# Optimization experiments

Measured on AMD Instinct MI355X. Metric: run time of the kernel, lower is better.

Reference implementation:

```python
import jax, jax.numpy as jnp
import numpy as np

DIM = 512
NUM_HEADS = 8
HEAD_DIM = DIM // NUM_HEADS


def setup_inputs() -> dict:
    key = jax.random.key(0)
    ks = jax.random.split(key, 9)
    s = 1.0 / np.sqrt(DIM)
    x = jax.random.normal(ks[0], (2, 4096, DIM), dtype=jnp.float32)
    Wq = jax.random.uniform(ks[1], (DIM, DIM), jnp.float32, -s, s)
    bq = jax.random.uniform(ks[2], (DIM,), jnp.float32, -s, s)
    Wk = jax.random.uniform(ks[3], (DIM, DIM), jnp.float32, -s, s)
    bk = jax.random.uniform(ks[4], (DIM,), jnp.float32, -s, s)
    Wv = jax.random.uniform(ks[5], (DIM, DIM), jnp.float32, -s, s)
    bv = jax.random.uniform(ks[6], (DIM,), jnp.float32, -s, s)
    Wo = jax.random.uniform(ks[7], (DIM, DIM), jnp.float32, -s, s)
    bo = jax.random.uniform(ks[8], (DIM,), jnp.float32, -s, s)
    return {"x": x, "Wq": Wq, "bq": bq, "Wk": Wk, "bk": bk,
            "Wv": Wv, "bv": bv, "Wo": Wo, "bo": bo}


def reference(x, Wq, bq, Wk, bk, Wv, bv, Wo, bo):
    B, S, D = x.shape
    H, Hd = NUM_HEADS, HEAD_DIM
    # Linear layers (torch stores weight as [out,in]; here W is [in,out])
    q = (x @ Wq + bq).reshape(B, S, H, Hd).transpose(0, 2, 1, 3)  # [B,H,S,Hd]
    k = (x @ Wk + bk).reshape(B, S, H, Hd).transpose(0, 2, 1, 3)
    v = (x @ Wv + bv).reshape(B, S, H, Hd).transpose(0, 2, 1, 3)
    # NOTE: original scales by dim**0.5, not head_dim**0.5
    energy = jnp.einsum('bhqd,bhkd->bhqk', q, k) / jnp.sqrt(jnp.float32(D))
    attn = jax.nn.softmax(energy, axis=-1)
    out = jnp.einsum('bhqk,bhkd->bhqd', attn, v)
    out = out.transpose(0, 2, 1, 3).reshape(B, S, D)
    return out @ Wo + bo
```

## Files before the change

kernel.cpp:

```cpp
#include <hip/hip_runtime.h>

typedef unsigned short USH;
typedef short s16x8 __attribute__((ext_vector_type(8)));
typedef float f32x4 __attribute__((ext_vector_type(4)));
typedef float f32x4v __attribute__((ext_vector_type(4)));
typedef unsigned int u32x4 __attribute__((ext_vector_type(4)));
typedef s16x8 s16x8_a __attribute__((may_alias));
typedef f32x4v f32x4v_a __attribute__((may_alias));
typedef u32x4 u32x4_a __attribute__((may_alias));
typedef unsigned long long u64_a __attribute__((may_alias));

#if __has_builtin(__builtin_amdgcn_exp2f)
#define EXP2F(x) __builtin_amdgcn_exp2f(x)
#else
#define EXP2F(x) __builtin_exp2f(x)
#endif

__device__ __forceinline__ USH f2bf(float f) {
  union { float f; unsigned int i; } c; c.f = f;
  unsigned int x = c.i;
  return (USH)((x + 0x7FFFu + ((x >> 16) & 1u)) >> 16);
}
__device__ __forceinline__ unsigned int pk_bf16(float a, float b) {
#if __has_builtin(__builtin_amdgcn_cvt_pk_bf16_f32)
  typedef USH ush2 __attribute__((ext_vector_type(2)));
  union { ush2 v; unsigned int u; } r;
  r.v = __builtin_amdgcn_cvt_pk_bf16_f32(a, b);
  return r.u;
#else
  union { float f; unsigned int i; } ca, cb; ca.f = a; cb.f = b;
  return ((ca.i + 0x8000u) >> 16) | ((cb.i + 0x8000u) & 0xFFFF0000u);
#endif
}

__device__ __forceinline__ f32x4 mfma16(s16x8 a, s16x8 b, f32x4 c) {
  return __builtin_amdgcn_mfma_f32_16x16x32_bf16(a, b, c, 0, 0, 0);
}

__global__ void transpose_w(const float* __restrict__ Wq, const float* __restrict__ Wk,
                            const float* __restrict__ Wv, const float* __restrict__ Wo,
                            USH* __restrict__ wsT) {
  __shared__ float tile[32][33];
  const int z = blockIdx.z;
  const float* W = (z == 0) ? Wq : (z == 1) ? Wk : (z == 2) ? Wv : Wo;
  USH* WT = wsT + (size_t)z * 262144;
  const int n0 = blockIdx.x * 32, k0 = blockIdx.y * 32;
  const int tx = threadIdx.x, ty = threadIdx.y;
  #pragma unroll
  for (int i = 0; i < 4; ++i)
    tile[ty + i * 8][tx] = W[(size_t)(k0 + ty + i * 8) * 512 + n0 + tx];
  __syncthreads();
  #pragma unroll
  for (int i = 0; i < 4; ++i)
    WT[(size_t)(n0 + ty + i * 8) * 512 + k0 + tx] = f2bf(tile[tx][ty + i * 8]);
}

__global__ __launch_bounds__(256) void cvt_x(const float* __restrict__ x,
                                             USH* __restrict__ xb) {
  const size_t i = ((size_t)blockIdx.x * 256 + threadIdx.x) * 8;
  const f32x4v a = *(const f32x4v_a*)(x + i);
  const f32x4v b = *(const f32x4v_a*)(x + i + 4);
  u32x4 s;
  s.x = pk_bf16(a.x, a.y); s.y = pk_bf16(a.z, a.w);
  s.z = pk_bf16(b.x, b.y); s.w = pk_bf16(b.z, b.w);
  *(u32x4_a*)(xb + i) = s;
}

template <int MODE>
__global__ __launch_bounds__(256, 3) void gemm_bias(
    const USH* __restrict__ A, const USH* __restrict__ BT0,
    const float* __restrict__ b0, const float* __restrict__ b1,
    const float* __restrict__ b2,
    USH* __restrict__ oQ, USH* __restrict__ oKV, float* __restrict__ oF) {
  __shared__ __align__(16) USH As[128 * 68];
  __shared__ __align__(16) USH Bs[128 * 68];
  const int z = blockIdx.z;
  const USH* BT = BT0 + (size_t)z * 262144;
  const float* bias = (z == 0) ? b0 : ((z == 1) ? b1 : b2);
  USH* outb = (z == 0) ? oQ : (oKV + (size_t)(z - 1) * 4194304);
  const float qs = (MODE == 1 && z == 0) ? 0.06375871528132839f : 1.0f;

  const int t = threadIdx.x;
  const int w = t >> 6, lane = t & 63;
  const int c = lane & 15, g = lane >> 4;
  const int wm = w & 1, wn = w >> 1;
  const int m0 = blockIdx.x * 128, n0 = blockIdx.y * 128;
  const int srow = t >> 1, scol = (t & 1) * 32;

  f32x4 acc[4][4] = {};

  const USH* Ap0 = A + (size_t)(m0 + srow) * 512 + scol;
  const USH* Bp0 = BT + (size_t)(n0 + srow) * 512 + scol;
  s16x8 pa[4], pb[4];
  #pragma unroll
  for (int j = 0; j < 4; ++j) {
    pa[j] = *(const s16x8_a*)(Ap0 + j * 8);
    pb[j] = *(const s16x8_a*)(Bp0 + j * 8);
  }

  for (int kt = 0; kt < 8; ++kt) {
    __syncthreads();
    #pragma unroll
    for (int j = 0; j < 4; ++j) {
      *(s16x8_a*)(As + srow * 68 + scol + j * 8) = pa[j];
      *(s16x8_a*)(Bs + srow * 68 + scol + j * 8) = pb[j];
    }
    const int ktn = (kt < 7) ? kt + 1 : kt;
    #pragma unroll
    for (int j = 0; j < 4; ++j) {
      pa[j] = *(const s16x8_a*)(Ap0 + ktn * 64 + j * 8);
      pb[j] = *(const s16x8_a*)(Bp0 + ktn * 64 + j * 8);
    }
    __syncthreads();
    #pragma unroll
    for (int ks = 0; ks < 2; ++ks) {
      s16x8 af[4], bfr[4];
      #pragma unroll
      for (int i = 0; i < 4; ++i) {
        af[i]  = *(const s16x8_a*)(As + (wm * 64 + i * 16 + c) * 68 + ks * 32 + g * 8);
        bfr[i] = *(const s16x8_a*)(Bs + (wn * 64 + i * 16 + c) * 68 + ks * 32 + g * 8);
      }
      #pragma unroll
      for (int mf = 0; mf < 4; ++mf)
        #pragma unroll
        for (int nf = 0; nf < 4; ++nf)
          acc[mf][nf] = mfma16(af[mf], bfr[nf], acc[mf][nf]);
    }
  }

  #pragma unroll
  for (int nf = 0; nf < 4; ++nf) {
    const int n = n0 + wn * 64 + nf * 16 + c;
    const float bv = bias[n];
    #pragma unroll
    for (int mf = 0; mf < 4; ++mf)
      #pragma unroll
      for (int r = 0; r < 4; ++r) {
        const int m = m0 + wm * 64 + mf * 16 + g * 4 + r;
        const float v = (acc[mf][nf][r] + bv) * qs;
        if (MODE == 0) {
          oF[(size_t)m * 512 + n] = v;
        } else {
          const int bb = m >> 12, s = m & 4095, h = n >> 6, hd = n & 63;
          if (z == 2)
            outb[(((size_t)(bb * 8 + h)) * 64 + hd) * 4096 + s] = f2bf(v);
          else
            outb[(((size_t)(bb * 8 + h)) * 4096 + s) * 64 + hd] = f2bf(v);
        }
      }
  }
}

__global__ __launch_bounds__(256, 2) void attn(const USH* __restrict__ Qbuf,
                                               const USH* __restrict__ kv,
                                               USH* __restrict__ att) {
  __shared__ __align__(16) USH Ks[2 * 64 * 36];
  __shared__ __align__(16) USH Ps[4][32 * 76];
  __shared__ float lbuf[4][32];

  const int t = threadIdx.x;
  const int w = t >> 6, lane = t & 63;
  const int c = lane & 15, g = lane >> 4;
  const int bh = blockIdx.y;
  const int bb = bh >> 3, hh = bh & 7;
  const size_t base = (size_t)bh * 262144;
  const USH* Q = Qbuf + base;
  const USH* K = kv + base;
  const USH* V = kv + 4194304 + base;
  const int q0 = blockIdx.x * 128 + w * 32;

  s16x8 qf[2][2];
  #pragma unroll
  for (int colf = 0; colf < 2; ++colf)
    #pragma unroll
    for (int kh = 0; kh < 2; ++kh)
      qf[colf][kh] = *(const s16x8_a*)(Q + (size_t)(q0 + colf * 16 + c) * 64 + kh * 32 + g * 8);

  s16x8 onesf;
  {
    const short one = (short)0x3F80, val = (c == 0) ? one : (short)0;
    #pragma unroll
    for (int j = 0; j < 8; ++j) onesf[j] = val;
  }

  f32x4 o[2][4] = {};
  f32x4 o_l[2] = {};
  const int kr = t >> 2, kc = (t & 3) * 16;
  const USH* Kp0 = K + (size_t)kr * 64 + kc;
  const int khalf = kc >> 5, koff = kc & 31;
  const USH* Vp = V + (size_t)c * 4096 + g * 8;

  s16x8 pk0 = *(const s16x8_a*)(Kp0);
  s16x8 pk1 = *(const s16x8_a*)(Kp0 + 8);
  s16x8 pv[2][4];
  #pragma unroll
  for (int kf = 0; kf < 2; ++kf)
    #pragma unroll
    for (int hf = 0; hf < 4; ++hf)
      pv[kf][hf] = *(const s16x8_a*)(Vp + (size_t)hf * 65536 + kf * 32);

  for (int kt = 0; kt < 64; ++kt) {
    __syncthreads();
    *(s16x8_a*)(Ks + khalf * 2304 + kr * 36 + koff) = pk0;
    *(s16x8_a*)(Ks + khalf * 2304 + kr * 36 + koff + 8) = pk1;
    const int ktn = (kt < 63) ? kt + 1 : kt;
    pk0 = *(const s16x8_a*)(Kp0 + (size_t)ktn * 4096);
    pk1 = *(const s16x8_a*)(Kp0 + (size_t)ktn * 4096 + 8);
    __syncthreads();

    f32x4 st[4][2] = {};
    #pragma unroll
    for (int kh = 0; kh < 2; ++kh) {
      s16x8 ak[4];
      #pragma unroll
      for (int kff = 0; kff < 4; ++kff)
        ak[kff] = *(const s16x8_a*)(Ks + kh * 2304 + (kff * 16 + c) * 36 + g * 8);
      #pragma unroll
      for (int kff = 0; kff < 4; ++kff)
        #pragma unroll
        for (int colf = 0; colf < 2; ++colf)
          st[kff][colf] = mfma16(ak[kff], qf[colf][kh], st[kff][colf]);
    }

    #pragma unroll
    for (int colf = 0; colf < 2; ++colf)
      #pragma unroll
      for (int kff = 0; kff < 4; ++kff)
        #pragma unroll
        for (int r = 0; r < 4; ++r)
          st[kff][colf][r] = EXP2F(st[kff][colf][r]);

    #pragma unroll
    for (int colf = 0; colf < 2; ++colf)
      #pragma unroll
      for (int kff = 0; kff < 4; ++kff) {
        const unsigned int lo = pk_bf16(st[kff][colf][0], st[kff][colf][1]);
        const unsigned int hi = pk_bf16(st[kff][colf][2], st[kff][colf][3]);
        const unsigned long long pk64 =
            (unsigned long long)lo | ((unsigned long long)hi << 32);
        *(u64_a*)(&Ps[w][(c + 16 * colf) * 76 + kff * 16 + g * 4]) = pk64;
      }

    #pragma unroll
    for (int kf = 0; kf < 2; ++kf) {
      s16x8 ap[2];
      #pragma unroll
      for (int mf = 0; mf < 2; ++mf)
        ap[mf] = *(const s16x8_a*)(&Ps[w][(mf * 16 + c) * 76 + kf * 32 + g * 8]);
      #pragma unroll
      for (int mf = 0; mf < 2; ++mf) {
        #pragma unroll
        for (int hf = 0; hf < 4; ++hf)
          o[mf][hf] = mfma16(ap[mf], pv[kf][hf], o[mf][hf]);
        o_l[mf] = mfma16(ap[mf], onesf, o_l[mf]);
      }
    }
    #pragma unroll
    for (int kf = 0; kf < 2; ++kf)
      #pragma unroll
      for (int hf = 0; hf < 4; ++hf)
        pv[kf][hf] = *(const s16x8_a*)(Vp + (size_t)hf * 65536 + ktn * 64 + kf * 32);
  }

  if (c == 0) {
    #pragma unroll
    for (int mf = 0; mf < 2; ++mf)
      #pragma unroll
      for (int r = 0; r < 4; ++r)
        lbuf[w][mf * 16 + g * 4 + r] = o_l[mf][r];
  }
  __syncthreads();

  #pragma unroll
  for (int mf = 0; mf < 2; ++mf)
    #pragma unroll
    for (int r = 0; r < 4; ++r) {
      const int ml = mf * 16 + g * 4 + r;
      const float linv = 1.0f / lbuf[w][ml];
      const int qrow = q0 + ml;
      #pragma unroll
      for (int hf = 0; hf < 4; ++hf) {
        const int hd = c + 16 * hf;
        att[((size_t)(bb * 4096 + qrow)) * 512 + hh * 64 + hd] =
            f2bf(o[mf][hf][r] * linv);
      }
    }
}

extern "C" void kernel_launch(void* const* d_in, const int* in_sizes, int n_in,
                              void* d_out, int out_size, void* d_ws, size_t ws_size,
                              hipStream_t stream) {
  (void)in_sizes; (void)n_in; (void)out_size; (void)ws_size;
  const float* x  = (const float*)d_in[0];
  const float* Wq = (const float*)d_in[1];
  const float* bq = (const float*)d_in[2];
  const float* Wk = (const float*)d_in[3];
  const float* bk = (const float*)d_in[4];
  const float* Wv = (const float*)d_in[5];
  const float* bv = (const float*)d_in[6];
  const float* Wo = (const float*)d_in[7];
  const float* bo = (const float*)d_in[8];
  USH* ws  = (USH*)d_ws;
  USH* wT  = ws;
  USH* kv  = ws + 1048576;
  USH* att = ws + 1048576 + 8388608;
  float* outF = (float*)d_out;
  USH* qscratch = (USH*)d_out;
  USH* xb = (USH*)d_out + 4194304;

  transpose_w<<<dim3(16, 16, 4), dim3(32, 8), 0, stream>>>(Wq, Wk, Wv, Wo, wT);
  cvt_x<<<2048, 256, 0, stream>>>(x, xb);
  gemm_bias<1><<<dim3(64, 4, 3), 256, 0, stream>>>(xb, wT, bq, bk, bv,
                                                   qscratch, kv, nullptr);
  attn<<<dim3(32, 16), 256, 0, stream>>>(qscratch, kv, att);
  gemm_bias<0><<<dim3(64, 4, 1), 256, 0, stream>>>(att, wT + 3 * 262144, bo, bo, bo,
                                                   nullptr, nullptr, outF);
}
```

Measured before the change: 248.6 us.

## Stage K and V tiles via direct global-to-LDS loads with double-buffered swizzled layout

Replaces the register-staged K loads and the per-wave direct global V loads with global_load_lds transfers into double-buffered, XOR-swizzled LDS tiles for both K and V. Each V tile is now fetched once per block and shared by all four waves instead of being loaded by every wave. It also removes one barrier per iteration. There is a risk: the single barrier with async LDS loads depends on the loads of the next buffer being complete or waited on at the next sync, and the extra LDS use may affect occupancy.

```diff
diff --git a/kernel.cpp b/kernel.cpp
--- a/kernel.cpp
+++ b/kernel.cpp
@@ -36,6 +36,23 @@
 __device__ __forceinline__ f32x4 mfma16(s16x8 a, s16x8 b, f32x4 c) {
   return __builtin_amdgcn_mfma_f32_16x16x32_bf16(a, b, c, 0, 0, 0);
 }
+
+#if __has_builtin(__builtin_amdgcn_global_load_lds)
+#define HAS_GLD 1
+__device__ __forceinline__ void gld_lds16(const USH* g, USH* l) {
+  __builtin_amdgcn_global_load_lds(
+      static_cast<const unsigned int __attribute__((address_space(1)))*>(
+          (const void __attribute__((address_space(1)))*)g),
+      static_cast<unsigned int __attribute__((address_space(3)))*>(
+          (void __attribute__((address_space(3)))*)l),
+      16, 0, 0);
+}
+#else
+#define HAS_GLD 0
+__device__ __forceinline__ void gld_lds16(const USH* g, USH* l) {
+  *(s16x8_a*)l = *(const s16x8_a*)g;
+}
+#endif
 
 __global__ void transpose_w(const float* __restrict__ Wq, const float* __restrict__ Wk,
                             const float* __restrict__ Wv, const float* __restrict__ Wo,
@@ -154,7 +171,8 @@
 __global__ __launch_bounds__(256, 2) void attn(const USH* __restrict__ Qbuf,
                                                const USH* __restrict__ kv,
                                                USH* __restrict__ att) {
-  __shared__ __align__(16) USH Ks[2 * 64 * 36];
+  __shared__ __align__(16) USH Ks[2 * 4096];
+  __shared__ __align__(16) USH Vt[2 * 4096];
   __shared__ __align__(16) USH Ps[4][32 * 76];
   __shared__ float lbuf[4][32];
 
@@ -185,36 +203,45 @@
 
   f32x4 o[2][4] = {};
   f32x4 o_l[2] = {};
-  const int kr = t >> 2, kc = (t & 3) * 16;
-  const USH* Kp0 = K + (size_t)kr * 64 + kc;
-  const int khalf = kc >> 5, koff = kc & 31;
-  const USH* Vp = V + (size_t)c * 4096 + g * 8;
-
-  s16x8 pk0 = *(const s16x8_a*)(Kp0);
-  s16x8 pk1 = *(const s16x8_a*)(Kp0 + 8);
-  s16x8 pv[2][4];
-  #pragma unroll
-  for (int kf = 0; kf < 2; ++kf)
-    #pragma unroll
-    for (int hf = 0; hf < 4; ++hf)
-      pv[kf][hf] = *(const s16x8_a*)(Vp + (size_t)hf * 65536 + kf * 32);
+
+  const int rK = w * 16 + (lane >> 2);
+  const int ccK = (lane & 3) ^ ((lane >> 3) & 3);
+  const USH* gK0 = K + (size_t)rK * 64 + ccK * 8;
+  const int hdV = w * 16 + (lane >> 3);
+  const int ccV = (lane & 7) ^ ((lane >> 3) & 7);
+  const USH* gV0 = V + (size_t)hdV * 4096 + ccV * 8;
+  const USH* gV1 = V + (size_t)(hdV + 8) * 4096 + ccV * 8;
+  USH* lK = Ks + w * 512 + lane * 8;
+  USH* lV = Vt + w * 1024 + lane * 8;
+
+  gld_lds16(gK0, lK);
+  gld_lds16(gK0 + 32, lK + 2048);
+  gld_lds16(gV0, lV);
+  gld_lds16(gV1, lV + 512);
 
   for (int kt = 0; kt < 64; ++kt) {
+    const int buf = kt & 1;
     __syncthreads();
-    *(s16x8_a*)(Ks + khalf * 2304 + kr * 36 + koff) = pk0;
-    *(s16x8_a*)(Ks + khalf * 2304 + kr * 36 + koff + 8) = pk1;
-    const int ktn = (kt < 63) ? kt + 1 : kt;
-    pk0 = *(const s16x8_a*)(Kp0 + (size_t)ktn * 4096);
-    pk1 = *(const s16x8_a*)(Kp0 + (size_t)ktn * 4096 + 8);
-    __syncthreads();
+    if (kt < 63) {
+      const int nb = (buf ^ 1) * 4096;
+      const size_t kof = (size_t)(kt + 1) * 4096;
+      const size_t vof = (size_t)(kt + 1) * 64;
+      gld_lds16(gK0 + kof, lK + nb);
+      gld_lds16(gK0 + 32 + kof, lK + nb + 2048);
+      gld_lds16(gV0 + vof, lV + nb);
+      gld_lds16(gV1 + vof, lV + nb + 512);
+    }
 
     f32x4 st[4][2] = {};
     #pragma unroll
     for (int kh = 0; kh < 2; ++kh) {
       s16x8 ak[4];
       #pragma unroll
-      for (int kff = 0; kff < 4; ++kff)
-        ak[kff] = *(const s16x8_a*)(Ks + kh * 2304 + (kff * 16 + c) * 36 + g * 8);
+      for (int kff = 0; kff < 4; ++kff) {
+        const int row = kff * 16 + c;
+        const int qsw = (g ^ ((c >> 1) & 3)) * 8;
+        ak[kff] = *(const s16x8_a*)(Ks + buf * 4096 + kh * 2048 + row * 32 + qsw);
+      }
       #pragma unroll
       for (int kff = 0; kff < 4; ++kff)
         #pragma unroll
@@ -243,23 +270,23 @@
 
     #pragma unroll
     for (int kf = 0; kf < 2; ++kf) {
-      s16x8 ap[2];
+      s16x8 ap[2], bv[4];
       #pragma unroll
       for (int mf = 0; mf < 2; ++mf)
         ap[mf] = *(const s16x8_a*)(&Ps[w][(mf * 16 + c) * 76 + kf * 32 + g * 8]);
+      #pragma unroll
+      for (int hf = 0; hf < 4; ++hf) {
+        const int qv = ((kf * 4 + g) ^ (c & 7)) * 8;
+        bv[hf] = *(const s16x8_a*)(Vt + buf * 4096 + (c + 16 * hf) * 64 + qv);
+      }
       #pragma unroll
       for (int mf = 0; mf < 2; ++mf) {
         #pragma unroll
         for (int hf = 0; hf < 4; ++hf)
-          o[mf][hf] = mfma16(ap[mf], pv[kf][hf], o[mf][hf]);
+          o[mf][hf] = mfma16(ap[mf], bv[hf], o[mf][hf]);
         o_l[mf] = mfma16(ap[mf], onesf, o_l[mf]);
       }
     }
-    #pragma unroll
-    for (int kf = 0; kf < 2; ++kf)
-      #pragma unroll
-      for (int hf = 0; hf < 4; ++hf)
-        pv[kf][hf] = *(const s16x8_a*)(Vp + (size_t)hf * 65536 + ktn * 64 + kf * 32);
   }
 
   if (c == 0) {
```

After: 213.6 us. 14.1% less time.
